# Kernel optimization log

Measured on AMD Instinct MI355X. Metric: run time of the kernel, lower is better.

## Reference

```python
import jax, jax.numpy as jnp
import numpy as np

NG, G = 256, 32          # num groups, pedestrians per group
E, H, MID, BN_EPS = 64, 64, 512, 1e-5
BOT = 32

def _bn(x, gamma, beta):
    # training-mode BatchNorm1d applied PER GROUP (axis=1 are the rows of
    # that group's pairwise batch), biased variance, eps=1e-5
    mean = jnp.mean(x, axis=1, keepdims=True)
    var = jnp.mean((x - mean) ** 2, axis=1, keepdims=True)
    return gamma * (x - mean) * jax.lax.rsqrt(var + BN_EPS) + beta

def setup_inputs() -> dict:
    key = jax.random.key(0)
    ks = jax.random.split(key, 8)
    B = NG * G
    starts = np.arange(NG, dtype=np.int64) * G
    seq_start_end = jnp.asarray(np.stack([starts, starts + G], axis=1))
    def lin(k, fi, fo):
        kw, kb = jax.random.split(k)
        lim = 1.0 / np.sqrt(fi)
        return (jax.random.uniform(kw, (fi, fo), jnp.float32, -lim, lim),
                jax.random.uniform(kb, (fo,), jnp.float32, -lim, lim))
    W_spatial, b_spatial = lin(ks[0], 2, E)
    W1, b1 = lin(ks[1], E + H, MID)
    W2, b2 = lin(ks[2], MID, BOT)
    return {
        'h_states': jax.random.normal(ks[3], (1, B, H), jnp.float32),
        'seq_start_end': seq_start_end,
        'end_pos': jax.random.normal(ks[4], (B, 2), jnp.float32),
        'W_spatial': W_spatial, 'b_spatial': b_spatial,
        'W1': W1, 'b1': b1,
        'gamma1': jnp.ones((MID,), jnp.float32), 'beta1': jnp.zeros((MID,), jnp.float32),
        'W2': W2, 'b2': b2,
        'gamma2': jnp.ones((BOT,), jnp.float32), 'beta2': jnp.zeros((BOT,), jnp.float32),
    }

def reference(h_states, seq_start_end, end_pos, W_spatial, b_spatial,
              W1, b1, gamma1, beta1, W2, b2, gamma2, beta2):
    B = end_pos.shape[0]
    ng = seq_start_end.shape[0]
    g = B // ng  # equal-size groups -> fully vectorized
    h = h_states.reshape(B, H).reshape(ng, g, H)
    pos = end_pos.reshape(ng, g, 2)
    # rel[n, i, j] = pos[n, j] - pos[n, i]  (matches repeat/tile in torch code)
    rel = pos[:, None, :, :] - pos[:, :, None, :]            # (ng, g, g, 2)
    emb = rel @ W_spatial + b_spatial                         # (ng, g, g, E)
    hb = jnp.broadcast_to(h[:, None, :, :], (ng, g, g, H))    # hidden of ped j
    x = jnp.concatenate([emb, hb], axis=-1).reshape(ng, g * g, E + H)
    x = jax.nn.relu(_bn(x @ W1 + b1, gamma1, beta1))          # (ng, g*g, 512)
    x = jax.nn.relu(_bn(x @ W2 + b2, gamma2, beta2))          # (ng, g*g, 32)
    pool = x.reshape(ng, g, g, BOT).max(axis=2)               # max over j
    return pool.reshape(B, BOT)
```

## Files before the change

kernel.cpp:

```cpp
#include <hip/hip_runtime.h>

#define GRP 32
#define HD 64
#define MIDD 512
#define LDSTR 520

#define WS_W1B_OFF 4096
#define WS_W2_OFF  (4096 + 65536)

typedef _Float16 half8 __attribute__((ext_vector_type(8)));
typedef float floatx4 __attribute__((ext_vector_type(4)));

__device__ inline half8 relu8(half8 x) {
    return __builtin_elementwise_max(x, (half8)(_Float16)0);
}

__launch_bounds__(512)
__global__ void prep(const float* __restrict__ Ws,
                     const float* __restrict__ W1,
                     const float* __restrict__ W2,
                     float* __restrict__ wsf) {
    const int b = blockIdx.x, t = threadIdx.x;
    _Float16* w1b = (_Float16*)((char*)wsf + WS_W1B_OFF);
    _Float16* w2f = (_Float16*)((char*)wsf + WS_W2_OFF);
    if (b == 0) {
        const int c = t;
        float p0[4] = {0.f, 0.f, 0.f, 0.f}, p1[4] = {0.f, 0.f, 0.f, 0.f};
#pragma unroll
        for (int e = 0; e < 64; e += 4) {
#pragma unroll
            for (int u = 0; u < 4; ++u) {
                float w = W1[(e + u) * MIDD + c];
                p0[u] = fmaf(Ws[e + u], w, p0[u]);
                p1[u] = fmaf(Ws[64 + e + u], w, p1[u]);
            }
        }
        wsf[c]       = (p0[0] + p0[1]) + (p0[2] + p0[3]);
        wsf[512 + c] = (p1[0] + p1[1]) + (p1[2] + p1[3]);
    } else if (b <= 8) {
        const int base = (b - 1) * 4096 + t * 8;
        const int fid = base >> 3;
        const int n16 = fid & 15, quad = (fid >> 4) & 3;
        const int kk = (fid >> 6) & 1, cblk = fid >> 7;
        const int c = cblk * 16 + n16;
#pragma unroll
        for (int x = 0; x < 8; ++x) {
            int k = kk * 32 + quad * 8 + x;
            w1b[base + x] = (_Float16)W1[(size_t)(64 + k) * MIDD + c];
        }
    } else {
        const int base0 = (b - 9) * 8192 + t * 16;
#pragma unroll
        for (int i = 0; i < 16; i += 8) {
            const int base = base0 + i;
            const int fid = base >> 3;
            const int n16 = fid & 15, quad = (fid >> 4) & 3;
            const int kk = (fid >> 6) & 15, nt = (fid >> 10) & 1;
#pragma unroll
            for (int x = 0; x < 8; ++x) {
                int k = kk * 32 + quad * 8 + x;
                w2f[base + x] = (_Float16)W2[(size_t)k * 32 + nt * 16 + n16];
            }
        }
    }
}

__launch_bounds__(512, 2)
__global__ void pool_all(const float* __restrict__ h_states,
                         const float* __restrict__ end_pos,
                         const float* __restrict__ wsf,
                         const float* __restrict__ gamma1,
                         const float* __restrict__ beta1,
                         const float* __restrict__ gamma2,
                         const float* __restrict__ beta2,
                         float* __restrict__ out) {
    __shared__ _Float16 Ash[32][LDSTR];
    __shared__ _Float16 Bsh[32][LDSTR];
    __shared__ half8 w2l8[2048];
    __shared__ float posx[32], posy[32];
    __shared__ float red[8][2][16][2];
    __shared__ float bns[32], bno[32];

    const int tid  = threadIdx.x;
    const int wave = tid >> 6;
    const int lane = tid & 63;
    const int quad = lane >> 4;
    const int n16  = lane & 15;
    const int g0   = blockIdx.x * GRP;

    const _Float16* w1bf = (const _Float16*)((const char*)wsf + WS_W1B_OFF);
    const _Float16* w2f  = (const _Float16*)((const char*)wsf + WS_W2_OFF);
    _Float16* w2l = (_Float16*)w2l8;

    if (tid < 32) {
        posx[tid] = end_pos[(g0 + tid) * 2];
        posy[tid] = end_pos[(g0 + tid) * 2 + 1];
    }

    {
        const float4* s4 = (const float4*)w2f;
        float4* d4 = (float4*)w2l8;
#pragma unroll
        for (int i = 0; i < 4; ++i) d4[tid + i * 512] = s4[tid + i * 512];
    }

    half8 afr[2][2];
#pragma unroll
    for (int mt = 0; mt < 2; ++mt)
#pragma unroll
        for (int kk = 0; kk < 2; ++kk) {
            const float4* hp = (const float4*)(h_states + (size_t)(g0 + mt * 16 + n16) * HD + kk * 32 + quad * 8);
            float4 p0 = hp[0], p1 = hp[1];
            half8 a;
            a[0] = (_Float16)p0.x; a[1] = (_Float16)p0.y; a[2] = (_Float16)p0.z; a[3] = (_Float16)p0.w;
            a[4] = (_Float16)p1.x; a[5] = (_Float16)p1.y; a[6] = (_Float16)p1.z; a[7] = (_Float16)p1.w;
            afr[mt][kk] = a;
        }

    half8 bc0, bc1;
    float wrc0, wrc1, g1c, b1c;
    {
        const int c0 = (wave * 4) * 16 + n16;
        bc0 = *(const half8*)&w1bf[(size_t)((((wave * 4) * 2 + 0) * 4 + quad) * 16 + n16) * 8];
        bc1 = *(const half8*)&w1bf[(size_t)((((wave * 4) * 2 + 1) * 4 + quad) * 16 + n16) * 8];
        wrc0 = wsf[c0]; wrc1 = wsf[512 + c0];
        g1c = gamma1[c0]; b1c = beta1[c0];
    }

    __syncthreads();

#pragma unroll 1
    for (int nt4 = 0; nt4 < 4; ++nt4) {
        const int nn = (nt4 + 1) & 3;
        const int cn = (wave * 4 + nn) * 16 + n16;
        half8 bn0 = *(const half8*)&w1bf[(size_t)((((wave * 4 + nn) * 2 + 0) * 4 + quad) * 16 + n16) * 8];
        half8 bn1 = *(const half8*)&w1bf[(size_t)((((wave * 4 + nn) * 2 + 1) * 4 + quad) * 16 + n16) * 8];
        float wrn0 = wsf[cn], wrn1 = wsf[512 + cn];
        float g1n = gamma1[cn], b1n = beta1[cn];

        const int c = (wave * 4 + nt4) * 16 + n16;

        floatx4 accm[2];
        accm[0] = (floatx4){0.f, 0.f, 0.f, 0.f};
        accm[1] = (floatx4){0.f, 0.f, 0.f, 0.f};
#pragma unroll
        for (int mt = 0; mt < 2; ++mt) {
            accm[mt] = __builtin_amdgcn_mfma_f32_16x16x32_f16(afr[mt][0], bc0, accm[mt], 0, 0, 0);
            accm[mt] = __builtin_amdgcn_mfma_f32_16x16x32_f16(afr[mt][1], bc1, accm[mt], 0, 0, 0);
        }

        const float w0 = wrc0, w1 = wrc1;

        float su = 0.f, ssu = 0.f;
#pragma unroll
        for (int mt = 0; mt < 2; ++mt)
#pragma unroll
            for (int r = 0; r < 4; ++r) {
                int j = mt * 16 + quad * 4 + r;
                float u = accm[mt][r] + posx[j] * w0 + posy[j] * w1;
                accm[mt][r] = u;
                su += u;
                ssu = fmaf(u, u, ssu);
            }
        su  += __shfl_xor(su, 16);  su  += __shfl_xor(su, 32);
        ssu += __shfl_xor(ssu, 16); ssu += __shfl_xor(ssu, 32);

        float vv[8];
        float sv = 0.f, ssv = 0.f;
#pragma unroll
        for (int ii = 0; ii < 8; ++ii) {
            int i = quad * 8 + ii;
            float v = posx[i] * w0 + posy[i] * w1;
            vv[ii] = v;
            sv += v;
            ssv = fmaf(v, v, ssv);
        }
        sv  += __shfl_xor(sv, 16);  sv  += __shfl_xor(sv, 32);
        ssv += __shfl_xor(ssv, 16); ssv += __shfl_xor(ssv, 32);

        const float muu = su * (1.f / 32.f), muv = sv * (1.f / 32.f);
        const float var = (ssu * (1.f / 32.f) - muu * muu) + (ssv * (1.f / 32.f) - muv * muv);
        const float s    = g1c * rsqrtf(var + 1e-5f);
        const float boff = s * (muu - muv) - b1c;

#pragma unroll
        for (int mt = 0; mt < 2; ++mt)
#pragma unroll
            for (int r = 0; r < 4; ++r) {
                int j = mt * 16 + quad * 4 + r;
                Ash[j][c] = (_Float16)(s * accm[mt][r]);
            }
#pragma unroll
        for (int ii = 0; ii < 8; ++ii)
            Bsh[quad * 8 + ii][c] = (_Float16)fmaf(s, vv[ii], boff);

        bc0 = bn0; bc1 = bn1;
        wrc0 = wrn0; wrc1 = wrn1;
        g1c = g1n; b1c = b1n;
    }
    __syncthreads();

    floatx4 acc2[8][2];
#pragma unroll
    for (int a = 0; a < 8; ++a)
#pragma unroll
        for (int b = 0; b < 2; ++b) acc2[a][b] = (floatx4){0.f, 0.f, 0.f, 0.f};

    const int ib = wave * 4;
    half8 pa0[2], pa1[2], pw0[2], pw1[2], pbf[2][4];

#define PREB(BUF, KK) {                                                        \
        const int kb_ = (KK) * 32 + quad * 8;                                  \
        pw0[BUF] = *(const half8*)&w2l[(size_t)(((KK) * 4 + quad) * 16 + n16) * 8];        \
        pw1[BUF] = *(const half8*)&w2l[(size_t)(((16 + (KK)) * 4 + quad) * 16 + n16) * 8]; \
        pa0[BUF] = *(const half8*)&Ash[n16][kb_];                              \
        pa1[BUF] = *(const half8*)&Ash[16 + n16][kb_];                         \
        pbf[BUF][0] = *(const half8*)&Bsh[ib + 0][kb_];                        \
        pbf[BUF][1] = *(const half8*)&Bsh[ib + 1][kb_];                        \
        pbf[BUF][2] = *(const half8*)&Bsh[ib + 2][kb_];                        \
        pbf[BUF][3] = *(const half8*)&Bsh[ib + 3][kb_];                        \
    }

#define COMPB(BUF) {                                                           \
        _Pragma("unroll")                                                      \
        for (int mp = 0; mp < 4; ++mp) {                                       \
            const half8 bf = pbf[BUF][mp];                                     \
            const half8 z0 = relu8(pa0[BUF] - bf);                             \
            const half8 z1 = relu8(pa1[BUF] - bf);                             \
            acc2[2 * mp][0]     = __builtin_amdgcn_mfma_f32_16x16x32_f16(z0, pw0[BUF], acc2[2 * mp][0], 0, 0, 0);     \
            acc2[2 * mp][1]     = __builtin_amdgcn_mfma_f32_16x16x32_f16(z0, pw1[BUF], acc2[2 * mp][1], 0, 0, 0);     \
            acc2[2 * mp + 1][0] = __builtin_amdgcn_mfma_f32_16x16x32_f16(z1, pw0[BUF], acc2[2 * mp + 1][0], 0, 0, 0); \
            acc2[2 * mp + 1][1] = __builtin_amdgcn_mfma_f32_16x16x32_f16(z1, pw1[BUF], acc2[2 * mp + 1][1], 0, 0, 0); \
        }                                                                      \
    }

    PREB(0, 0)
#pragma unroll 1
    for (int t = 0; t < 7; ++t) {
        const int k1 = 2 * t + 1, k2 = 2 * t + 2;
        PREB(1, k1)
        COMPB(0)
        PREB(0, k2)
        COMPB(1)
    }
    PREB(1, 15)
    COMPB(0)
    COMPB(1)

#undef PREB
#undef COMPB

    float s0 = 0.f, q0 = 0.f, s1 = 0.f, q1 = 0.f;
#pragma unroll
    for (int mt = 0; mt < 8; ++mt)
#pragma unroll
        for (int r = 0; r < 4; ++r) {
            float v0 = acc2[mt][0][r], v1 = acc2[mt][1][r];
            s0 += v0; q0 = fmaf(v0, v0, q0);
            s1 += v1; q1 = fmaf(v1, v1, q1);
        }
    s0 += __shfl_xor(s0, 16); s0 += __shfl_xor(s0, 32);
    q0 += __shfl_xor(q0, 16); q0 += __shfl_xor(q0, 32);
    s1 += __shfl_xor(s1, 16); s1 += __shfl_xor(s1, 32);
    q1 += __shfl_xor(q1, 16); q1 += __shfl_xor(q1, 32);
    if (lane < 16) {
        red[wave][0][lane][0] = s0; red[wave][0][lane][1] = q0;
        red[wave][1][lane][0] = s1; red[wave][1][lane][1] = q1;
    }
    __syncthreads();
    if (tid < 32) {
        const int nt = tid >> 4, n = tid & 15;
        float s = 0.f, q = 0.f;
#pragma unroll
        for (int w = 0; w < 8; ++w) { s += red[w][nt][n][0]; q += red[w][nt][n][1]; }
        const float mu  = s * (1.f / 1024.f);
        const float var = q * (1.f / 1024.f) - mu * mu;
        const float sc  = gamma2[tid] * rsqrtf(var + 1e-5f);
        bns[tid] = sc;
        bno[tid] = beta2[tid] - sc * mu;
    }
    __syncthreads();

#pragma unroll
    for (int nt = 0; nt < 2; ++nt) {
        const int c = nt * 16 + n16;
        const float sc = bns[c], off = bno[c];
#pragma unroll
        for (int a = 0; a < 4; ++a) {
            float m = 0.f;
#pragma unroll
            for (int p = 0; p < 2; ++p)
#pragma unroll
                for (int r = 0; r < 4; ++r)
                    m = fmaxf(m, fmaf(sc, acc2[2 * a + p][nt][r], off));
            m = fmaxf(m, __shfl_xor(m, 16));
            m = fmaxf(m, __shfl_xor(m, 32));
            if (quad == nt) {
                const int i = wave * 4 + a;
                out[(size_t)(g0 + i) * 32 + c] = m;
            }
        }
    }
}

extern "C" void kernel_launch(void* const* d_in, const int* in_sizes, int n_in,
                              void* d_out, int out_size, void* d_ws, size_t ws_size,
                              hipStream_t stream) {
    (void)in_sizes; (void)n_in; (void)out_size; (void)ws_size;
    const float* h_states  = (const float*)d_in[0];
    const float* end_pos   = (const float*)d_in[2];
    const float* W_spatial = (const float*)d_in[3];
    const float* W1        = (const float*)d_in[5];
    const float* gamma1    = (const float*)d_in[7];
    const float* beta1     = (const float*)d_in[8];
    const float* W2        = (const float*)d_in[9];
    const float* gamma2    = (const float*)d_in[11];
    const float* beta2     = (const float*)d_in[12];
    float* out = (float*)d_out;
    float* wsf = (float*)d_ws;

    prep<<<dim3(11), dim3(512), 0, stream>>>(W_spatial, W1, W2, wsf);
    pool_all<<<dim3(256), dim3(512), 0, stream>>>(h_states, end_pos, wsf,
                                                  gamma1, beta1, gamma2, beta2, out);
}
```

Before: 97.30 us.

## Split each group across two blocks and finish BN2 with a separate kernel

Each group's work is now split over two 256-thread blocks, each handling half of the i rows. Both blocks still recompute the full layer-1 output for their group. Each block writes partial BN2 sums plus per-row max/min of the pre-BN values to workspace, and a third kernel combines them, applying the scale/offset by choosing max or min according to the sign of the scale. W2 fragments are held in registers instead of LDS, and the explicit double-buffered prefetch is replaced by a fully unrolled loop. This doubles the block count for better CU occupancy, at the cost of duplicated layer-1 work, an extra launch, and higher register pressure.

```diff
diff --git a/kernel.cpp b/kernel.cpp
--- a/kernel.cpp
+++ b/kernel.cpp
@@ -7,6 +7,8 @@
 
 #define WS_W1B_OFF 4096
 #define WS_W2_OFF  (4096 + 65536)
+#define WS_STAT_F  ((4096 + 65536 + 32768) / 4)
+#define WS_MXMN_F  (WS_STAT_F + 512 * 64)
 
 typedef _Float16 half8 __attribute__((ext_vector_type(8)));
 typedef float floatx4 __attribute__((ext_vector_type(4)));
@@ -65,43 +67,39 @@
     }
 }
 
-__launch_bounds__(512, 2)
-__global__ void pool_all(const float* __restrict__ h_states,
-                         const float* __restrict__ end_pos,
-                         const float* __restrict__ wsf,
-                         const float* __restrict__ gamma1,
-                         const float* __restrict__ beta1,
-                         const float* __restrict__ gamma2,
-                         const float* __restrict__ beta2,
-                         float* __restrict__ out) {
+__launch_bounds__(256, 2)
+__global__ void pool_main(const float* __restrict__ h_states,
+                          const float* __restrict__ end_pos,
+                          float* __restrict__ wsf,
+                          const float* __restrict__ gamma1,
+                          const float* __restrict__ beta1) {
     __shared__ _Float16 Ash[32][LDSTR];
-    __shared__ _Float16 Bsh[32][LDSTR];
-    __shared__ half8 w2l8[2048];
+    __shared__ _Float16 Bsh[16][LDSTR];
     __shared__ float posx[32], posy[32];
-    __shared__ float red[8][2][16][2];
-    __shared__ float bns[32], bno[32];
+    __shared__ float red[4][2][16][2];
 
     const int tid  = threadIdx.x;
     const int wave = tid >> 6;
     const int lane = tid & 63;
     const int quad = lane >> 4;
     const int n16  = lane & 15;
-    const int g0   = blockIdx.x * GRP;
+    const int n    = blockIdx.x >> 1;
+    const int p    = blockIdx.x & 1;
+    const int g0   = n * GRP;
 
     const _Float16* w1bf = (const _Float16*)((const char*)wsf + WS_W1B_OFF);
     const _Float16* w2f  = (const _Float16*)((const char*)wsf + WS_W2_OFF);
-    _Float16* w2l = (_Float16*)w2l8;
 
     if (tid < 32) {
         posx[tid] = end_pos[(g0 + tid) * 2];
         posy[tid] = end_pos[(g0 + tid) * 2 + 1];
     }
 
-    {
-        const float4* s4 = (const float4*)w2f;
-        float4* d4 = (float4*)w2l8;
-#pragma unroll
-        for (int i = 0; i < 4; ++i) d4[tid + i * 512] = s4[tid + i * 512];
+    half8 w2a[16], w2b[16];
+#pragma unroll
+    for (int kk = 0; kk < 16; ++kk) {
+        w2a[kk] = *(const half8*)&w2f[(size_t)((kk * 4 + quad) * 16 + n16) * 8];
+        w2b[kk] = *(const half8*)&w2f[(size_t)(((16 + kk) * 4 + quad) * 16 + n16) * 8];
     }
 
     half8 afr[2][2];
@@ -120,9 +118,10 @@
     half8 bc0, bc1;
     float wrc0, wrc1, g1c, b1c;
     {
-        const int c0 = (wave * 4) * 16 + n16;
-        bc0 = *(const half8*)&w1bf[(size_t)((((wave * 4) * 2 + 0) * 4 + quad) * 16 + n16) * 8];
-        bc1 = *(const half8*)&w1bf[(size_t)((((wave * 4) * 2 + 1) * 4 + quad) * 16 + n16) * 8];
+        const int cb0 = wave * 8;
+        const int c0 = cb0 * 16 + n16;
+        bc0 = *(const half8*)&w1bf[(size_t)(((cb0 * 2 + 0) * 4 + quad) * 16 + n16) * 8];
+        bc1 = *(const half8*)&w1bf[(size_t)(((cb0 * 2 + 1) * 4 + quad) * 16 + n16) * 8];
         wrc0 = wsf[c0]; wrc1 = wsf[512 + c0];
         g1c = gamma1[c0]; b1c = beta1[c0];
     }
@@ -130,15 +129,16 @@
     __syncthreads();
 
 #pragma unroll 1
-    for (int nt4 = 0; nt4 < 4; ++nt4) {
-        const int nn = (nt4 + 1) & 3;
-        const int cn = (wave * 4 + nn) * 16 + n16;
-        half8 bn0 = *(const half8*)&w1bf[(size_t)((((wave * 4 + nn) * 2 + 0) * 4 + quad) * 16 + n16) * 8];
-        half8 bn1 = *(const half8*)&w1bf[(size_t)((((wave * 4 + nn) * 2 + 1) * 4 + quad) * 16 + n16) * 8];
+    for (int t = 0; t < 8; ++t) {
+        const int nn = (t + 1) & 7;
+        const int cbn = wave * 8 + nn;
+        const int cn = cbn * 16 + n16;
+        half8 bn0 = *(const half8*)&w1bf[(size_t)(((cbn * 2 + 0) * 4 + quad) * 16 + n16) * 8];
+        half8 bn1 = *(const half8*)&w1bf[(size_t)(((cbn * 2 + 1) * 4 + quad) * 16 + n16) * 8];
         float wrn0 = wsf[cn], wrn1 = wsf[512 + cn];
         float g1n = gamma1[cn], b1n = beta1[cn];
 
-        const int c = (wave * 4 + nt4) * 16 + n16;
+        const int c = (wave * 8 + t) * 16 + n16;
 
         floatx4 accm[2];
         accm[0] = (floatx4){0.f, 0.f, 0.f, 0.f};
@@ -190,9 +190,11 @@
                 int j = mt * 16 + quad * 4 + r;
                 Ash[j][c] = (_Float16)(s * accm[mt][r]);
             }
-#pragma unroll
-        for (int ii = 0; ii < 8; ++ii)
-            Bsh[quad * 8 + ii][c] = (_Float16)fmaf(s, vv[ii], boff);
+        if ((quad >> 1) == p) {
+#pragma unroll
+            for (int ii = 0; ii < 8; ++ii)
+                Bsh[(quad & 1) * 8 + ii][c] = (_Float16)fmaf(s, vv[ii], boff);
+        }
 
         bc0 = bn0; bc1 = bn1;
         wrc0 = wrn0; wrc1 = wrn1;
@@ -206,49 +208,23 @@
 #pragma unroll
         for (int b = 0; b < 2; ++b) acc2[a][b] = (floatx4){0.f, 0.f, 0.f, 0.f};
 
-    const int ib = wave * 4;
-    half8 pa0[2], pa1[2], pw0[2], pw1[2], pbf[2][4];
-
-#define PREB(BUF, KK) {                                                        \
-        const int kb_ = (KK) * 32 + quad * 8;                                  \
-        pw0[BUF] = *(const half8*)&w2l[(size_t)(((KK) * 4 + quad) * 16 + n16) * 8];        \
-        pw1[BUF] = *(const half8*)&w2l[(size_t)(((16 + (KK)) * 4 + quad) * 16 + n16) * 8]; \
-        pa0[BUF] = *(const half8*)&Ash[n16][kb_];                              \
-        pa1[BUF] = *(const half8*)&Ash[16 + n16][kb_];                         \
-        pbf[BUF][0] = *(const half8*)&Bsh[ib + 0][kb_];                        \
-        pbf[BUF][1] = *(const half8*)&Bsh[ib + 1][kb_];                        \
-        pbf[BUF][2] = *(const half8*)&Bsh[ib + 2][kb_];                        \
-        pbf[BUF][3] = *(const half8*)&Bsh[ib + 3][kb_];                        \
-    }
-
-#define COMPB(BUF) {                                                           \
-        _Pragma("unroll")                                                      \
-        for (int mp = 0; mp < 4; ++mp) {                                       \
-            const half8 bf = pbf[BUF][mp];                                     \
-            const half8 z0 = relu8(pa0[BUF] - bf);                             \
-            const half8 z1 = relu8(pa1[BUF] - bf);                             \
-            acc2[2 * mp][0]     = __builtin_amdgcn_mfma_f32_16x16x32_f16(z0, pw0[BUF], acc2[2 * mp][0], 0, 0, 0);     \
-            acc2[2 * mp][1]     = __builtin_amdgcn_mfma_f32_16x16x32_f16(z0, pw1[BUF], acc2[2 * mp][1], 0, 0, 0);     \
-            acc2[2 * mp + 1][0] = __builtin_amdgcn_mfma_f32_16x16x32_f16(z1, pw0[BUF], acc2[2 * mp + 1][0], 0, 0, 0); \
-            acc2[2 * mp + 1][1] = __builtin_amdgcn_mfma_f32_16x16x32_f16(z1, pw1[BUF], acc2[2 * mp + 1][1], 0, 0, 0); \
-        }                                                                      \
-    }
-
-    PREB(0, 0)
-#pragma unroll 1
-    for (int t = 0; t < 7; ++t) {
-        const int k1 = 2 * t + 1, k2 = 2 * t + 2;
-        PREB(1, k1)
-        COMPB(0)
-        PREB(0, k2)
-        COMPB(1)
-    }
-    PREB(1, 15)
-    COMPB(0)
-    COMPB(1)
-
-#undef PREB
-#undef COMPB
+    const int ibl = wave * 4;
+#pragma unroll
+    for (int kk = 0; kk < 16; ++kk) {
+        const int kb = kk * 32 + quad * 8;
+        const half8 a0 = *(const half8*)&Ash[n16][kb];
+        const half8 a1 = *(const half8*)&Ash[16 + n16][kb];
+#pragma unroll
+        for (int mp = 0; mp < 4; ++mp) {
+            const half8 bf = *(const half8*)&Bsh[ibl + mp][kb];
+            const half8 z0 = relu8(a0 - bf);
+            const half8 z1 = relu8(a1 - bf);
+            acc2[2 * mp][0]     = __builtin_amdgcn_mfma_f32_16x16x32_f16(z0, w2a[kk], acc2[2 * mp][0], 0, 0, 0);
+            acc2[2 * mp][1]     = __builtin_amdgcn_mfma_f32_16x16x32_f16(z0, w2b[kk], acc2[2 * mp][1], 0, 0, 0);
+            acc2[2 * mp + 1][0] = __builtin_amdgcn_mfma_f32_16x16x32_f16(z1, w2a[kk], acc2[2 * mp + 1][0], 0, 0, 0);
+            acc2[2 * mp + 1][1] = __builtin_amdgcn_mfma_f32_16x16x32_f16(z1, w2b[kk], acc2[2 * mp + 1][1], 0, 0, 0);
+        }
+    }
 
     float s0 = 0.f, q0 = 0.f, s1 = 0.f, q1 = 0.f;
 #pragma unroll
@@ -269,37 +245,70 @@
     }
     __syncthreads();
     if (tid < 32) {
-        const int nt = tid >> 4, n = tid & 15;
+        const int nt = tid >> 4, nc = tid & 15;
         float s = 0.f, q = 0.f;
 #pragma unroll
-        for (int w = 0; w < 8; ++w) { s += red[w][nt][n][0]; q += red[w][nt][n][1]; }
+        for (int w = 0; w < 4; ++w) { s += red[w][nt][nc][0]; q += red[w][nt][nc][1]; }
+        wsf[WS_STAT_F + blockIdx.x * 64 + tid]      = s;
+        wsf[WS_STAT_F + blockIdx.x * 64 + 32 + tid] = q;
+    }
+
+#pragma unroll
+    for (int nt = 0; nt < 2; ++nt) {
+        const int c = nt * 16 + n16;
+#pragma unroll
+        for (int a = 0; a < 4; ++a) {
+            float mx = -3.402823466e38f, mn = 3.402823466e38f;
+#pragma unroll
+            for (int p2 = 0; p2 < 2; ++p2)
+#pragma unroll
+                for (int r = 0; r < 4; ++r) {
+                    float v = acc2[2 * a + p2][nt][r];
+                    mx = fmaxf(mx, v);
+                    mn = fminf(mn, v);
+                }
+            mx = fmaxf(mx, __shfl_xor(mx, 16));
+            mx = fmaxf(mx, __shfl_xor(mx, 32));
+            mn = fminf(mn, __shfl_xor(mn, 16));
+            mn = fminf(mn, __shfl_xor(mn, 32));
+            if (quad == nt) {
+                const int il = wave * 4 + a;
+                const int base = WS_MXMN_F + ((blockIdx.x * 16 + il) * 32 + c) * 2;
+                wsf[base]     = mx;
+                wsf[base + 1] = mn;
+            }
+        }
+    }
+}
+
+__launch_bounds__(128)
+__global__ void pool_fin(const float* __restrict__ wsf,
+                         const float* __restrict__ gamma2,
+                         const float* __restrict__ beta2,
+                         float* __restrict__ out) {
+    __shared__ float scs[32], offs[32];
+    const int tid = threadIdx.x, n = blockIdx.x, g0 = n * GRP;
+    if (tid < 32) {
+        const int c = tid;
+        float s = wsf[WS_STAT_F + (2 * n) * 64 + c]      + wsf[WS_STAT_F + (2 * n + 1) * 64 + c];
+        float q = wsf[WS_STAT_F + (2 * n) * 64 + 32 + c] + wsf[WS_STAT_F + (2 * n + 1) * 64 + 32 + c];
         const float mu  = s * (1.f / 1024.f);
         const float var = q * (1.f / 1024.f) - mu * mu;
-        const float sc  = gamma2[tid] * rsqrtf(var + 1e-5f);
-        bns[tid] = sc;
-        bno[tid] = beta2[tid] - sc * mu;
+        const float sc  = gamma2[c] * rsqrtf(var + 1e-5f);
+        scs[c]  = sc;
+        offs[c] = beta2[c] - sc * mu;
     }
     __syncthreads();
-
-#pragma unroll
-    for (int nt = 0; nt < 2; ++nt) {
-        const int c = nt * 16 + n16;
-        const float sc = bns[c], off = bno[c];
-#pragma unroll
-        for (int a = 0; a < 4; ++a) {
-            float m = 0.f;
-#pragma unroll
-            for (int p = 0; p < 2; ++p)
-#pragma unroll
-                for (int r = 0; r < 4; ++r)
-                    m = fmaxf(m, fmaf(sc, acc2[2 * a + p][nt][r], off));
-            m = fmaxf(m, __shfl_xor(m, 16));
-            m = fmaxf(m, __shfl_xor(m, 32));
-            if (quad == nt) {
-                const int i = wave * 4 + a;
-                out[(size_t)(g0 + i) * 32 + c] = m;
-            }
-        }
+#pragma unroll
+    for (int k = 0; k < 8; ++k) {
+        const int idx = tid + k * 128;
+        const int i = idx >> 5, c = idx & 31;
+        const int blk = n * 2 + (i >> 4), il = i & 15;
+        const int base = WS_MXMN_F + ((blk * 16 + il) * 32 + c) * 2;
+        const float mx = wsf[base], mn = wsf[base + 1];
+        const float sc = scs[c];
+        const float v = (sc >= 0.f) ? mx : mn;
+        out[(size_t)(g0 + i) * 32 + c] = fmaxf(0.f, fmaf(sc, v, offs[c]));
     }
 }
 
@@ -320,6 +329,6 @@
     float* wsf = (float*)d_ws;
 
     prep<<<dim3(11), dim3(512), 0, stream>>>(W_spatial, W1, W2, wsf);
-    pool_all<<<dim3(256), dim3(512), 0, stream>>>(h_states, end_pos, wsf,
-                                                  gamma1, beta1, gamma2, beta2, out);
-}
+    pool_main<<<dim3(512), dim3(256), 0, stream>>>(h_states, end_pos, wsf, gamma1, beta1);
+    pool_fin<<<dim3(256), dim3(128), 0, stream>>>(wsf, gamma2, beta2, out);
+}
```

Result: slower. 104.3 us (+7.2%).
